# Kernel optimization log

Measured on AMD Instinct MI355X. Metric: run time of the kernel, lower is better.

Reference implementation:

```python
import jax, jax.numpy as jnp
import numpy as np

B, DM, H, W = 4, 192, 48, 48
DI = 2 * DM          # d_inner = d_expand (ssm_ratio=ssm_rank_ratio=2)
K, N, R = 4, 16, 12  # directions, d_state, dt_rank=ceil(192/16)
L = H * W
EPS = 1e-5


def setup_inputs() -> dict:
    key = jax.random.key(0)
    ks = jax.random.split(key, 10)
    f = lambda k, s, sc: (sc * jax.random.normal(k, s)).astype(jnp.float32)
    return {
        "x": jax.random.normal(ks[0], (B, DM, H, W), jnp.float32),
        "in_proj_w": f(ks[1], (2 * DI, DM), 0.05),        # Conv2d 1x1, bias=False
        "conv_w": f(ks[2], (DI, 1, 3, 3), 0.1),           # depthwise 3x3
        "conv_b": f(ks[3], (DI,), 0.1),
        "x_proj_weight": f(ks[4], (K, R + 2 * N, DI), 0.05),
        "dt_projs_weight": f(ks[5], (K, DI, R), 0.1),
        "dt_projs_bias": f(ks[6], (K, DI), 0.5),
        "A_logs": f(ks[7], (K * DI, N), 0.5),
        "Ds": jnp.ones((K * DI,), jnp.float32),
        "ln_w": jnp.ones((DI,), jnp.float32),
        "ln_b": jnp.zeros((DI,), jnp.float32),
        "out_proj_w": f(ks[8], (DM, DI), 0.05),           # Conv2d 1x1, bias=False
    }


def selective_scan(u, delta, A, Bs, Cs, Ds):
    # u, delta: (B,K,D,L); A: (K,D,N); Bs, Cs: (B,K,N,L); Ds: (K,D)
    uT = jnp.moveaxis(u, -1, 0)
    dT = jnp.moveaxis(delta, -1, 0)
    BT = jnp.moveaxis(Bs, -1, 0)
    CT = jnp.moveaxis(Cs, -1, 0)
    h0 = jnp.zeros(u.shape[:3] + (A.shape[-1],), u.dtype)  # (B,K,D,N)

    def step(h, inp):
        u_l, d_l, B_l, C_l = inp  # (B,K,D),(B,K,D),(B,K,N),(B,K,N)
        dA = jnp.exp(d_l[..., None] * A)                    # (B,K,D,N)
        h = h * dA + (d_l * u_l)[..., None] * B_l[:, :, None, :]
        y = jnp.einsum("bkdn,bkn->bkd", h, C_l)
        return h, y

    _, ys = jax.lax.scan(step, h0, (uT, dT, BT, CT))       # ys: (L,B,K,D)
    ys = jnp.moveaxis(ys, 0, -1)                            # (B,K,D,L)
    return ys + u * Ds[None, :, :, None]


def _forward(x, in_proj_w, conv_w, conv_b, x_proj_weight, dt_projs_weight,
             dt_projs_bias, A_logs, Ds, ln_w, ln_b, out_proj_w):
    # in_proj (1x1 conv) -> split x / z; z branch gets exact GELU
    xz = jnp.einsum("od,bdhw->bohw", in_proj_w, x)
    xc, z = jnp.split(xz, 2, axis=1)
    z1 = jax.nn.gelu(z, approximate=False)
    # depthwise 3x3 conv + GELU
    xc = jax.lax.conv_general_dilated(
        xc, conv_w, (1, 1), "SAME",
        feature_group_count=DI,
        dimension_numbers=("NCHW", "OIHW", "NCHW"),
    ) + conv_b[None, :, None, None]
    xc = jax.nn.gelu(xc, approximate=False)
    # CrossScan: row-major, col-major, and their reversals -> (B,K,D,L)
    x0 = xc.reshape(B, DI, L)
    x1 = jnp.swapaxes(xc, 2, 3).reshape(B, DI, L)
    xs = jnp.stack([x0, x1, x0[..., ::-1], x1[..., ::-1]], axis=1)
    # per-direction projections
    x_dbl = jnp.einsum("bkdl,kcd->bkcl", xs, x_proj_weight)
    dts, Bs, Cs = jnp.split(x_dbl, [R, R + N], axis=2)      # (B,K,R,L),(B,K,N,L)x2
    dts = jnp.einsum("bkrl,kdr->bkdl", dts, dt_projs_weight)
    delta = jax.nn.softplus(dts + dt_projs_bias[None, :, :, None])
    A = -jnp.exp(A_logs.reshape(K, DI, N))
    ys = selective_scan(xs, delta, A, Bs, Cs, Ds.reshape(K, DI))
    # CrossMerge: un-flip, fold col-major branch back to row-major
    y02 = ys[:, 0] + ys[:, 2, :, ::-1]
    y13 = ys[:, 1] + ys[:, 3, :, ::-1]
    y = y02 + jnp.swapaxes(y13.reshape(B, DI, W, H), 2, 3).reshape(B, DI, L)
    # out_norm (LayerNorm over channel) in (B,H,W,D)
    y = y.reshape(B, DI, H, W).transpose(0, 2, 3, 1)
    mu = y.mean(-1, keepdims=True)
    var = ((y - mu) ** 2).mean(-1, keepdims=True)
    y = (y - mu) / jnp.sqrt(var + EPS) * ln_w + ln_b
    # gate with z, out_proj 1x1
    y = y.transpose(0, 3, 1, 2) * z1
    return jnp.einsum("od,bdhw->bohw", out_proj_w, y)


def reference(x, in_proj_w, conv_w, conv_b, x_proj_weight, dt_projs_weight,
              dt_projs_bias, A_logs, Ds, ln_w, ln_b, out_proj_w):
    return _forward(x, in_proj_w, conv_w, conv_b, x_proj_weight,
                    dt_projs_weight, dt_projs_bias, A_logs, Ds,
                    ln_w, ln_b, out_proj_w)
```

## Files before the change

kernel.cpp:

```cpp
#include <hip/hip_runtime.h>
#include <math.h>

#define BQ 4
#define DM 192
#define DI 384
#define HH 48
#define WW 48
#define LL 2304
#define KK 4
#define NN 16
#define RR 12
#define CH 48
#define CLEN 48

#define LOG2E 1.4426950408889634f

typedef short v8s __attribute__((ext_vector_type(8)));
typedef float v4f __attribute__((ext_vector_type(4)));

__device__ __forceinline__ float gelu_exact(float x) {
    return 0.5f * x * (1.0f + erff(x * 0.7071067811865476f));
}

__device__ __forceinline__ float softplus_f(float x) {
    return fmaxf(x, 0.0f) + log1pf(expf(-fabsf(x)));
}

__device__ __forceinline__ int pos_for(int k, int l) {
    if (k == 0) return l;
    if (k == 1) { return (l % HH) * WW + (l / HH); }
    if (k == 2) return (LL - 1) - l;
    int j = (LL - 1) - l;
    return (j % HH) * WW + (j / HH);
}

__device__ __forceinline__ int pt_of(int p) {
    return (p % 48) * 48 + p / 48;
}

__device__ __forceinline__ float fexp2(float x) {
    return __builtin_amdgcn_exp2f(x);
}

__device__ __forceinline__ short f2bf(float x) {
    unsigned u = __float_as_uint(x);
    unsigned r = (u + 0x7FFFu + ((u >> 16) & 1u)) >> 16;
    return (short)r;
}

template<int CTRL>
__device__ __forceinline__ float dpp_movf(float v) {
    return __int_as_float(__builtin_amdgcn_update_dpp(
        0, __float_as_int(v), CTRL, 0xF, 0xF, true));
}

__global__ __launch_bounds__(256) void k_prep_w(const float* __restrict__ ipw,
                                                const float* __restrict__ opw,
                                                const float* __restrict__ xpw,
                                                short* __restrict__ wibf,
                                                short* __restrict__ owbf,
                                                short* __restrict__ wpbf) {
    int i = blockIdx.x * 256 + threadIdx.x;
    if (i < 147456)       wibf[i] = f2bf(ipw[i]);
    else if (i < 221184)  owbf[i - 147456] = f2bf(opw[i - 147456]);
    else if (i < 288768)  wpbf[i - 221184] = f2bf(xpw[i - 221184]);
    else                  wpbf[67584 + (i - 288768)] = 0;
}

__global__ __launch_bounds__(256) void k_prep_xT(const float* __restrict__ x,
                                                 short* __restrict__ xTbf) {
    __shared__ float T[32][33];
    int blk = blockIdx.x;
    int dt = blk % 6;
    int lt = (blk / 6) % 72;
    int b  = blk / (6 * 72);
    int d0 = dt * 32, l0 = lt * 32;
    int tx = threadIdx.x & 31, ty = threadIdx.x >> 5;
    #pragma unroll
    for (int i = 0; i < 4; ++i) {
        int dd = ty + 8 * i;
        T[dd][tx] = x[(size_t)(b * DM + d0 + dd) * LL + l0 + tx];
    }
    __syncthreads();
    #pragma unroll
    for (int i = 0; i < 4; ++i) {
        int ll = ty + 8 * i;
        xTbf[(size_t)(b * LL + l0 + ll) * DM + d0 + tx] = f2bf(T[tx][ll]);
    }
}

__global__ __launch_bounds__(256) void k_inproj_mfma(
    const short* __restrict__ xTbf,
    const short* __restrict__ wibf,
    float* __restrict__ xcz)
{
    __shared__ short sA[128 * 40];
    __shared__ short sB[64 * 40];
    int o0 = blockIdx.x * 64;
    int l0 = blockIdx.y * 128;
    int b  = blockIdx.z;
    int tid = threadIdx.x;
    int lane = tid & 63, wid = tid >> 6;
    int n = lane & 15, quad = lane >> 4;

    v4f acc[2][4];
    #pragma unroll
    for (int i = 0; i < 2; ++i)
        #pragma unroll
        for (int j = 0; j < 4; ++j) acc[i][j] = (v4f){0.f, 0.f, 0.f, 0.f};

    for (int kc = 0; kc < 192; kc += 32) {
        for (int i = tid; i < 512; i += 256) {
            int row = i >> 2, seg = i & 3;
            *(v8s*)&sA[row * 40 + seg * 8] =
                *(const v8s*)(xTbf + (size_t)(b * LL + l0 + row) * DM + kc + seg * 8);
        }
        {
            int row = tid >> 2, seg = tid & 3;
            *(v8s*)&sB[row * 40 + seg * 8] =
                *(const v8s*)(wibf + (size_t)(o0 + row) * DM + kc + seg * 8);
        }
        __syncthreads();
        v8s a0 = *(v8s*)&sA[(wid * 32 + n) * 40 + quad * 8];
        v8s a1 = *(v8s*)&sA[(wid * 32 + 16 + n) * 40 + quad * 8];
        #pragma unroll
        for (int os = 0; os < 4; ++os) {
            v8s bv = *(v8s*)&sB[(os * 16 + n) * 40 + quad * 8];
            acc[0][os] = __builtin_amdgcn_mfma_f32_16x16x32_bf16(a0, bv, acc[0][os], 0, 0, 0);
            acc[1][os] = __builtin_amdgcn_mfma_f32_16x16x32_bf16(a1, bv, acc[1][os], 0, 0, 0);
        }
        __syncthreads();
    }
    bool zhalf = (o0 >= DI);
    #pragma unroll
    for (int ls = 0; ls < 2; ++ls)
        #pragma unroll
        for (int os = 0; os < 4; ++os) {
            int o = o0 + os * 16 + n;
            #pragma unroll
            for (int r = 0; r < 4; ++r) {
                int l = l0 + wid * 32 + ls * 16 + quad * 4 + r;
                float v = acc[ls][os][r];
                xcz[(size_t)(b * LL + l) * 768 + o] = zhalf ? gelu_exact(v) : v;
            }
        }
}

__global__ __launch_bounds__(384) void k_dwconv(const float* __restrict__ xcz,
                                                const float* __restrict__ cw,
                                                const float* __restrict__ cb,
                                                float* __restrict__ xcT,
                                                short* __restrict__ xcTbf) {
    int blk = blockIdx.x;
    int seg = blk & 3;
    int bh = blk >> 2;
    int b = bh / HH, h = bh % HH;
    int d = threadIdx.x;
    int w0 = seg * 12;
    const float* in = xcz + (size_t)b * LL * 768 + d;
    float w9[9];
    #pragma unroll
    for (int i = 0; i < 9; ++i) w9[i] = cw[d * 9 + i];
    float bias = cb[d];
    bool hm = h > 0, hp = h < HH - 1;
    int r0 = (h - 1) * WW, r1 = h * WW, r2 = (h + 1) * WW;
    float c00, c01, c02, c10, c11, c12, c20, c21, c22;
    bool wl = (w0 > 0);
    c00 = (hm && wl) ? in[(size_t)(r0 + w0 - 1) * 768] : 0.f;
    c10 = wl ? in[(size_t)(r1 + w0 - 1) * 768] : 0.f;
    c20 = (hp && wl) ? in[(size_t)(r2 + w0 - 1) * 768] : 0.f;
    c01 = hm ? in[(size_t)(r0 + w0) * 768] : 0.f;
    c11 = in[(size_t)(r1 + w0) * 768];
    c21 = hp ? in[(size_t)(r2 + w0) * 768] : 0.f;
    c02 = hm ? in[(size_t)(r0 + w0 + 1) * 768] : 0.f;
    c12 = in[(size_t)(r1 + w0 + 1) * 768];
    c22 = hp ? in[(size_t)(r2 + w0 + 1) * 768] : 0.f;
    #pragma unroll
    for (int wi = 0; wi < 12; ++wi) {
        int w = w0 + wi;
        float s = bias
            + w9[0] * c00 + w9[1] * c01 + w9[2] * c02
            + w9[3] * c10 + w9[4] * c11 + w9[5] * c12
            + w9[6] * c20 + w9[7] * c21 + w9[8] * c22;
        float v = gelu_exact(s);
        size_t row = (size_t)(b * LL + h * WW + w);
        xcT[row * DI + d] = v;
        xcTbf[row * DI + d] = f2bf(v);
        c00 = c01; c01 = c02; c10 = c11; c11 = c12; c20 = c21; c21 = c22;
        int wn = w + 2;
        bool okw = wn < WW;
        c02 = (hm && okw) ? in[(size_t)(r0 + wn) * 768] : 0.f;
        c12 = okw ? in[(size_t)(r1 + wn) * 768] : 0.f;
        c22 = (hp && okw) ? in[(size_t)(r2 + wn) * 768] : 0.f;
    }
}

__global__ __launch_bounds__(256) void k_xproj_mfma(
    const short* __restrict__ xcTbf,
    const short* __restrict__ wpbf,
    float* __restrict__ dts,
    float* __restrict__ Bsb,
    float* __restrict__ Csb)
{
    __shared__ short sA[128 * 40];
    __shared__ short sB[64 * 40];
    int o0 = blockIdx.x * 64;
    int l0 = blockIdx.y * 128;
    int b  = blockIdx.z;
    int tid = threadIdx.x;
    int lane = tid & 63, wid = tid >> 6;
    int n = lane & 15, quad = lane >> 4;

    v4f acc[2][4];
    #pragma unroll
    for (int i = 0; i < 2; ++i)
        #pragma unroll
        for (int j = 0; j < 4; ++j) acc[i][j] = (v4f){0.f, 0.f, 0.f, 0.f};

    for (int kc = 0; kc < DI; kc += 32) {
        for (int i = tid; i < 512; i += 256) {
            int row = i >> 2, seg = i & 3;
            *(v8s*)&sA[row * 40 + seg * 8] =
                *(const v8s*)(xcTbf + (size_t)(b * LL + l0 + row) * DI + kc + seg * 8);
        }
        {
            int row = tid >> 2, seg = tid & 3;
            *(v8s*)&sB[row * 40 + seg * 8] =
                *(const v8s*)(wpbf + (size_t)(o0 + row) * DI + kc + seg * 8);
        }
        __syncthreads();
        v8s a0 = *(v8s*)&sA[(wid * 32 + n) * 40 + quad * 8];
        v8s a1 = *(v8s*)&sA[(wid * 32 + 16 + n) * 40 + quad * 8];
        #pragma unroll
        for (int os = 0; os < 4; ++os) {
            v8s bv = *(v8s*)&sB[(os * 16 + n) * 40 + quad * 8];
            acc[0][os] = __builtin_amdgcn_mfma_f32_16x16x32_bf16(a0, bv, acc[0][os], 0, 0, 0);
            acc[1][os] = __builtin_amdgcn_mfma_f32_16x16x32_bf16(a1, bv, acc[1][os], 0, 0, 0);
        }
        __syncthreads();
    }
    #pragma unroll
    for (int ls = 0; ls < 2; ++ls)
        #pragma unroll
        for (int os = 0; os < 4; ++os) {
            int c_all = o0 + os * 16 + n;
            if (c_all >= 176) continue;
            int k = c_all / 44;
            int c = c_all - k * 44;
            int bk = b * 4 + k;
            #pragma unroll
            for (int r = 0; r < 4; ++r) {
                int lp = l0 + wid * 32 + ls * 16 + quad * 4 + r;
                int lk = (k == 0) ? lp
                       : (k == 1) ? pt_of(lp)
                       : (k == 2) ? (LL - 1 - lp)
                                  : (LL - 1 - pt_of(lp));
                float v = acc[ls][os][r];
                size_t base = (size_t)bk * LL + lk;
                if (c < RR)           dts[base * RR + c] = v;
                else if (c < RR + NN) Bsb[base * NN + (c - RR)] = v;
                else                  Csb[base * NN + (c - RR - NN)] = v;
            }
        }
}

__global__ __launch_bounds__(256) void k_scan_pass1(
    const float* __restrict__ xcT,
    const float* __restrict__ dts,
    const float* __restrict__ Bsb,
    const float* __restrict__ Csb,
    const float* __restrict__ dtw_g,
    const float* __restrict__ dtb_g,
    const float* __restrict__ Alogs,
    const float* __restrict__ Ds_g,
    float* __restrict__ Sbuf,
    float* __restrict__ hstin,
    float* __restrict__ yk)
{
    __shared__ float sB[CLEN * 16];
    __shared__ float sC[CLEN * 16];
    __shared__ float sDts[CLEN * 12];
    __shared__ float sDel[CLEN * 64];
    __shared__ float sU[CLEN * 64];

    int blk = blockIdx.x;
    int dblk = blk % 6;
    int tmp = blk / 6;
    int c = tmp % CH;
    int bk = tmp / CH;
    int k = bk & 3, b = bk >> 2;
    int tid = threadIdx.x;
    int l0 = c * CLEN;

    {
        const float4* Bg = (const float4*)(Bsb + ((size_t)bk * LL + l0) * NN);
        const float4* Cg = (const float4*)(Csb + ((size_t)bk * LL + l0) * NN);
        if (tid < CLEN * 4) {
            ((float4*)sB)[tid] = Bg[tid];
            ((float4*)sC)[tid] = Cg[tid];
        }
        const float4* Dg = (const float4*)(dts + ((size_t)bk * LL + l0) * RR);
        for (int i = tid; i < CLEN * 3; i += 256)
            ((float4*)sDts)[i] = Dg[i];
    }
    {
        const float* xb = xcT + (size_t)b * LL * DI + dblk * 64;
        #pragma unroll
        for (int it = 0; it < 3; ++it) {
            int i = it * 256 + tid;
            int l = i >> 4, f4 = i & 15;
            int pos = pos_for(k, l0 + l);
            ((float4*)sU)[l * 16 + f4] = *(const float4*)(xb + (size_t)pos * DI + f4 * 4);
        }
    }
    __syncthreads();
    {
        int dl = tid & 63, lset = tid >> 6;
        int dd = dblk * 64 + dl;
        int kdq = k * DI + dd;
        float dtbv = dtb_g[kdq];
        float w12[12];
        {
            const float4* p = (const float4*)(dtw_g + (size_t)kdq * RR);
            float4 a0 = p[0], a1 = p[1], a2 = p[2];
            w12[0]=a0.x; w12[1]=a0.y; w12[2]=a0.z;  w12[3]=a0.w;
            w12[4]=a1.x; w12[5]=a1.y; w12[6]=a1.z;  w12[7]=a1.w;
            w12[8]=a2.x; w12[9]=a2.y; w12[10]=a2.z; w12[11]=a2.w;
        }
        #pragma unroll
        for (int j = 0; j < 12; ++j) {
            int l = lset * 12 + j;
            const float* dp = sDts + l * 12;
            float acc = dtbv;
            #pragma unroll
            for (int r = 0; r < 12; ++r) acc += dp[r] * w12[r];
            sDel[l * 64 + dl] = softplus_f(acc);
        }
    }
    __syncthreads();

    int lane = tid & 63, wv = tid >> 6;
    int q = lane & 3;
    int d16 = lane >> 2;
    int dl = wv * 16 + d16;
    int d = dblk * 64 + dl;
    int kd = k * DI + d;
    int n0 = q << 2;

    float4 Al = *(const float4*)(Alogs + (size_t)kd * NN + n0);
    float A2[4] = { -expf(Al.x) * LOG2E, -expf(Al.y) * LOG2E,
                    -expf(Al.z) * LOG2E, -expf(Al.w) * LOG2E };
    float Dv = Ds_g[kd];
    float* Sc = Sbuf + ((size_t)bk * LL + l0 + q) * DI + d;
    float* yc = yk   + ((size_t)bk * LL + l0 + q) * DI + d;

    float h0 = 0.f, h1 = 0.f, h2 = 0.f, h3 = 0.f;
    float td = 0.f;
    float yhold = 0.f, Shold = 0.f;

    #pragma unroll
    for (int l = 0; l < CLEN; ++l) {
        float delta = sDel[l * 64 + dl];
        float ub_b  = sU[l * 64 + dl];
        td += delta;
        float du = delta * ub_b;
        float4 B4 = *(const float4*)&sB[l * 16 + n0];
        h0 = h0 * fexp2(delta * A2[0]) + du * B4.x;
        h1 = h1 * fexp2(delta * A2[1]) + du * B4.y;
        h2 = h2 * fexp2(delta * A2[2]) + du * B4.z;
        h3 = h3 * fexp2(delta * A2[3]) + du * B4.w;
        float4 C4 = *(const float4*)&sC[l * 16 + n0];
        float yp = h0 * C4.x + h1 * C4.y + h2 * C4.z + h3 * C4.w;
        yp += dpp_movf<0xB1>(yp);
        yp += dpp_movf<0x4E>(yp);
        float yf = yp + ub_b * Dv;
        if (q == (l & 3)) { yhold = yf; Shold = td; }
        if ((l & 3) == 3) {
            *yc = yhold; *Sc = Shold;
            yc += 4 * DI; Sc += 4 * DI;
        }
    }

    float4 h4; h4.x = h0; h4.y = h1; h4.z = h2; h4.w = h3;
    *(float4*)(hstin + ((size_t)(bk * CH + c) * DI + d) * NN + n0) = h4;
}

__global__ __launch_bounds__(256) void k_scan_combine(
    float* __restrict__ hstin,
    const float* __restrict__ Sbuf,
    const float* __restrict__ Alogs)
{
    int t = blockIdx.x * 256 + threadIdx.x;
    int n = t & 15;
    int d = (t >> 4) % DI;
    int bk = t / (DI * NN);
    int k = bk & 3;
    float A2 = -expf(Alogs[(size_t)(k * DI + d) * NN + n]) * LOG2E;
    float h = 0.f;
    for (int c = 0; c < CH; ++c) {
        size_t rb = (size_t)(bk * CH + c) * DI + d;
        float hend = hstin[rb * NN + n];
        hstin[rb * NN + n] = h;
        float St = Sbuf[((size_t)bk * LL + c * CLEN + CLEN - 1) * DI + d];
        h = fexp2(A2 * St) * h + hend;
    }
}

__global__ __launch_bounds__(256) void k_corr(
    const float* __restrict__ Csb,
    const float* __restrict__ Sbuf,
    const float* __restrict__ hin,
    const float* __restrict__ Alogs,
    float* __restrict__ yk)
{
    __shared__ float sC[CLEN * 16];
    __shared__ float sS[CLEN * 64];

    int blk = blockIdx.x;
    int dblk = blk % 6;
    int tmp = blk / 6;
    int c = tmp % CH;
    if (c == 0) return;
    int bk = tmp / CH;
    int k = bk & 3;
    int tid = threadIdx.x;
    int l0 = c * CLEN;

    {
        const float4* Cg = (const float4*)(Csb + ((size_t)bk * LL + l0) * NN);
        if (tid < CLEN * 4) ((float4*)sC)[tid] = Cg[tid];
        const float* Sg = Sbuf + ((size_t)bk * LL + l0) * DI + dblk * 64;
        #pragma unroll
        for (int it = 0; it < 3; ++it) {
            int i = it * 256 + tid;
            int l = i >> 4, f4 = i & 15;
            ((float4*)sS)[l * 16 + f4] = *(const float4*)(Sg + (size_t)l * DI + f4 * 4);
        }
    }
    __syncthreads();

    int lane = tid & 63, wv = tid >> 6;
    int q = lane & 3;
    int d16 = lane >> 2;
    int dl = wv * 16 + d16;
    int d = dblk * 64 + dl;
    int kd = k * DI + d;
    int n0 = q << 2;

    float4 Al = *(const float4*)(Alogs + (size_t)kd * NN + n0);
    float A2[4] = { -expf(Al.x) * LOG2E, -expf(Al.y) * LOG2E,
                    -expf(Al.z) * LOG2E, -expf(Al.w) * LOG2E };
    float4 H4 = *(const float4*)(hin + ((size_t)(bk * CH + c) * DI + d) * NN + n0);
    float* yc = yk + ((size_t)bk * LL + l0 + q) * DI + d;

    float ychold = 0.f;
    #pragma unroll
    for (int l = 0; l < CLEN; ++l) {
        float S = sS[l * 64 + dl];
        float4 C4 = *(const float4*)&sC[l * 16 + n0];
        float yv = C4.x * fexp2(A2[0] * S) * H4.x
                 + C4.y * fexp2(A2[1] * S) * H4.y
                 + C4.z * fexp2(A2[2] * S) * H4.z
                 + C4.w * fexp2(A2[3] * S) * H4.w;
        yv += dpp_movf<0xB1>(yv);
        yv += dpp_movf<0x4E>(yv);
        if (q == (l & 3)) ychold = yv;
        if ((l & 3) == 3) {
            *yc += ychold;
            yc += 4 * DI;
        }
    }
}

__global__ __launch_bounds__(384) void k_merge_ln_gate(
    const float* __restrict__ yk,
    const float* __restrict__ xcz,
    const float* __restrict__ lnw,
    const float* __restrict__ lnb,
    short* __restrict__ gbufb)
{
    int pg = blockIdx.x;
    int b = pg / LL;
    int pos = pg % LL;
    int d = threadIdx.x;
    int pt = (pos % 48) * 48 + pos / 48;

    const float* y0 = yk + ((size_t)(b * 4 + 0) * LL + pos) * DI;
    const float* y1 = yk + ((size_t)(b * 4 + 1) * LL + pt) * DI;
    const float* y2 = yk + ((size_t)(b * 4 + 2) * LL + (LL - 1 - pos)) * DI;
    const float* y3 = yk + ((size_t)(b * 4 + 3) * LL + (LL - 1 - pt)) * DI;
    float v = y0[d] + y1[d] + y2[d] + y3[d];

    float s = v, qq = v * v;
    #pragma unroll
    for (int o = 32; o >= 1; o >>= 1) {
        s += __shfl_xor(s, o, 64);
        qq += __shfl_xor(qq, o, 64);
    }
    __shared__ float ssum[6], sqq[6];
    int lane = d & 63, w = d >> 6;
    if (lane == 0) { ssum[w] = s; sqq[w] = qq; }
    __syncthreads();
    float ts = 0.f, tq = 0.f;
    #pragma unroll
    for (int i = 0; i < 6; ++i) { ts += ssum[i]; tq += sqq[i]; }
    float mu = ts / (float)DI;
    float var = tq / (float)DI - mu * mu;
    float inv = rsqrtf(var + 1e-5f);
    float y = (v - mu) * inv * lnw[d] + lnb[d];
    float z = xcz[(size_t)pg * 768 + DI + d];
    gbufb[(size_t)pg * DI + d] = f2bf(y * z);
}

__global__ __launch_bounds__(256) void k_outproj_mfma(
    const short* __restrict__ gbufb,
    const short* __restrict__ owbf,
    float* __restrict__ out)
{
    __shared__ short sA[128 * 40];
    __shared__ short sB[64 * 40];
    int o0 = blockIdx.x * 64;
    int l0 = blockIdx.y * 128;
    int b  = blockIdx.z;
    int tid = threadIdx.x;
    int lane = tid & 63, wid = tid >> 6;
    int n = lane & 15, quad = lane >> 4;

    v4f acc[2][4];
    #pragma unroll
    for (int i = 0; i < 2; ++i)
        #pragma unroll
        for (int j = 0; j < 4; ++j) acc[i][j] = (v4f){0.f, 0.f, 0.f, 0.f};

    for (int kc = 0; kc < DI; kc += 32) {
        for (int i = tid; i < 512; i += 256) {
            int row = i >> 2, seg = i & 3;
            *(v8s*)&sA[row * 40 + seg * 8] =
                *(const v8s*)(gbufb + (size_t)(b * LL + l0 + row) * DI + kc + seg * 8);
        }
        {
            int row = tid >> 2, seg = tid & 3;
            *(v8s*)&sB[row * 40 + seg * 8] =
                *(const v8s*)(owbf + (size_t)(o0 + row) * DI + kc + seg * 8);
        }
        __syncthreads();
        v8s a0 = *(v8s*)&sA[(wid * 32 + n) * 40 + quad * 8];
        v8s a1 = *(v8s*)&sA[(wid * 32 + 16 + n) * 40 + quad * 8];
        #pragma unroll
        for (int os = 0; os < 4; ++os) {
            v8s bv = *(v8s*)&sB[(os * 16 + n) * 40 + quad * 8];
            acc[0][os] = __builtin_amdgcn_mfma_f32_16x16x32_bf16(a0, bv, acc[0][os], 0, 0, 0);
            acc[1][os] = __builtin_amdgcn_mfma_f32_16x16x32_bf16(a1, bv, acc[1][os], 0, 0, 0);
        }
        __syncthreads();
    }
    #pragma unroll
    for (int ls = 0; ls < 2; ++ls)
        #pragma unroll
        for (int os = 0; os < 4; ++os) {
            int o = o0 + os * 16 + n;
            #pragma unroll
            for (int r = 0; r < 4; ++r) {
                int l = l0 + wid * 32 + ls * 16 + quad * 4 + r;
                out[(size_t)(b * DM + o) * LL + l] = acc[ls][os][r];
            }
        }
}

extern "C" void kernel_launch(void* const* d_in, const int* in_sizes, int n_in,
                              void* d_out, int out_size, void* d_ws, size_t ws_size,
                              hipStream_t stream) {
    (void)in_sizes; (void)n_in; (void)out_size; (void)ws_size;
    const float* x      = (const float*)d_in[0];
    const float* ipw    = (const float*)d_in[1];
    const float* cw     = (const float*)d_in[2];
    const float* cb     = (const float*)d_in[3];
    const float* xpw    = (const float*)d_in[4];
    const float* dtw    = (const float*)d_in[5];
    const float* dtb    = (const float*)d_in[6];
    const float* Alogs  = (const float*)d_in[7];
    const float* Ds     = (const float*)d_in[8];
    const float* lnw    = (const float*)d_in[9];
    const float* lnb    = (const float*)d_in[10];
    const float* opw    = (const float*)d_in[11];
    float* out = (float*)d_out;

    float* wsf = (float*)d_ws;
    const size_t XCZ = (size_t)BQ * LL * 768;
    const size_t SZ  = (size_t)BQ * DI * LL;
    const size_t DTS = (size_t)BQ * KK * LL * RR;
    const size_t BCS = (size_t)BQ * KK * LL * NN;
    const size_t SBF = (size_t)BQ * KK * LL * DI;
    const size_t HST = (size_t)BQ * KK * CH * DI * NN;

    float* xcz   = wsf;
    float* xcT   = xcz + XCZ;
    float* dts   = xcT + SZ;
    float* Bsb   = dts + DTS;
    float* Csb   = Bsb + BCS;
    float* Sbuf  = Csb + BCS;
    float* hstin = Sbuf + SBF;
    float* yk    = hstin + HST;
    short* xTbf  = (short*)(yk + SBF);
    short* wibf  = xTbf + (size_t)BQ * LL * DM;
    short* owbf  = wibf + 768 * 192;
    short* wpbf  = owbf + 192 * 384;
    short* gbufb = (short*)Sbuf;
    short* xcTbf = (short*)yk;

    k_prep_w<<<1152, 256, 0, stream>>>(ipw, opw, xpw, wibf, owbf, wpbf);
    k_prep_xT<<<BQ * 72 * 6, 256, 0, stream>>>(x, xTbf);
    k_inproj_mfma<<<dim3(12, 18, BQ), 256, 0, stream>>>(xTbf, wibf, xcz);
    k_dwconv<<<BQ * HH * 4, 384, 0, stream>>>(xcz, cw, cb, xcT, xcTbf);
    k_xproj_mfma<<<dim3(3, 18, BQ), 256, 0, stream>>>(xcTbf, wpbf, dts, Bsb, Csb);

    k_scan_pass1<<<BQ * KK * CH * 6, 256, 0, stream>>>(
        xcT, dts, Bsb, Csb, dtw, dtb, Alogs, Ds, Sbuf, hstin, yk);
    k_scan_combine<<<(BQ * KK * DI * NN) / 256, 256, 0, stream>>>(
        hstin, Sbuf, Alogs);
    k_corr<<<BQ * KK * CH * 6, 256, 0, stream>>>(Csb, Sbuf, hstin, Alogs, yk);
    k_merge_ln_gate<<<BQ * LL, 384, 0, stream>>>(yk, xcz, lnw, lnb, gbufb);

    k_outproj_mfma<<<dim3(3, 18, BQ), 256, 0, stream>>>(gbufb, owbf, out);
}
```

Before: 304.2 us.

## Recompute delta prefix sums in correction pass instead of storing full S buffer

The scan pass no longer writes the per-position cumulative delta buffer (B*K*L*DI floats). It stores only each chunk's final sum, which the combine kernel reads. The correction kernel instead reloads the small dt rows, recomputes delta via the dt projection and softplus, and keeps a running sum, trading a large global write and read for extra compute. The two prep kernels are also merged into one launch to save a kernel launch.

```diff
diff --git a/kernel.cpp b/kernel.cpp
--- a/kernel.cpp
+++ b/kernel.cpp
@@ -54,23 +54,24 @@
         0, __float_as_int(v), CTRL, 0xF, 0xF, true));
 }
 
-__global__ __launch_bounds__(256) void k_prep_w(const float* __restrict__ ipw,
-                                                const float* __restrict__ opw,
-                                                const float* __restrict__ xpw,
-                                                short* __restrict__ wibf,
-                                                short* __restrict__ owbf,
-                                                short* __restrict__ wpbf) {
-    int i = blockIdx.x * 256 + threadIdx.x;
-    if (i < 147456)       wibf[i] = f2bf(ipw[i]);
-    else if (i < 221184)  owbf[i - 147456] = f2bf(opw[i - 147456]);
-    else if (i < 288768)  wpbf[i - 221184] = f2bf(xpw[i - 221184]);
-    else                  wpbf[67584 + (i - 288768)] = 0;
-}
-
-__global__ __launch_bounds__(256) void k_prep_xT(const float* __restrict__ x,
-                                                 short* __restrict__ xTbf) {
+__global__ __launch_bounds__(256) void k_prep(const float* __restrict__ ipw,
+                                              const float* __restrict__ opw,
+                                              const float* __restrict__ xpw,
+                                              const float* __restrict__ x,
+                                              short* __restrict__ wibf,
+                                              short* __restrict__ owbf,
+                                              short* __restrict__ wpbf,
+                                              short* __restrict__ xTbf) {
     __shared__ float T[32][33];
-    int blk = blockIdx.x;
+    if (blockIdx.x < 1152) {
+        int i = blockIdx.x * 256 + threadIdx.x;
+        if (i < 147456)       wibf[i] = f2bf(ipw[i]);
+        else if (i < 221184)  owbf[i - 147456] = f2bf(opw[i - 147456]);
+        else if (i < 288768)  wpbf[i - 221184] = f2bf(xpw[i - 221184]);
+        else                  wpbf[67584 + (i - 288768)] = 0;
+        return;
+    }
+    int blk = blockIdx.x - 1152;
     int dt = blk % 6;
     int lt = (blk / 6) % 72;
     int b  = blk / (6 * 72);
@@ -273,7 +274,7 @@
     const float* __restrict__ dtb_g,
     const float* __restrict__ Alogs,
     const float* __restrict__ Ds_g,
-    float* __restrict__ Sbuf,
+    float* __restrict__ Sfin,
     float* __restrict__ hstin,
     float* __restrict__ yk)
 {
@@ -351,12 +352,11 @@
     float A2[4] = { -expf(Al.x) * LOG2E, -expf(Al.y) * LOG2E,
                     -expf(Al.z) * LOG2E, -expf(Al.w) * LOG2E };
     float Dv = Ds_g[kd];
-    float* Sc = Sbuf + ((size_t)bk * LL + l0 + q) * DI + d;
-    float* yc = yk   + ((size_t)bk * LL + l0 + q) * DI + d;
+    float* yc = yk + ((size_t)bk * LL + l0 + q) * DI + d;
 
     float h0 = 0.f, h1 = 0.f, h2 = 0.f, h3 = 0.f;
     float td = 0.f;
-    float yhold = 0.f, Shold = 0.f;
+    float yhold = 0.f;
 
     #pragma unroll
     for (int l = 0; l < CLEN; ++l) {
@@ -374,20 +374,21 @@
         yp += dpp_movf<0xB1>(yp);
         yp += dpp_movf<0x4E>(yp);
         float yf = yp + ub_b * Dv;
-        if (q == (l & 3)) { yhold = yf; Shold = td; }
+        if (q == (l & 3)) yhold = yf;
         if ((l & 3) == 3) {
-            *yc = yhold; *Sc = Shold;
-            yc += 4 * DI; Sc += 4 * DI;
+            *yc = yhold;
+            yc += 4 * DI;
         }
     }
 
     float4 h4; h4.x = h0; h4.y = h1; h4.z = h2; h4.w = h3;
     *(float4*)(hstin + ((size_t)(bk * CH + c) * DI + d) * NN + n0) = h4;
+    if (q == 0) Sfin[(size_t)(bk * CH + c) * DI + d] = td;
 }
 
 __global__ __launch_bounds__(256) void k_scan_combine(
     float* __restrict__ hstin,
-    const float* __restrict__ Sbuf,
+    const float* __restrict__ Sfin,
     const float* __restrict__ Alogs)
 {
     int t = blockIdx.x * 256 + threadIdx.x;
@@ -401,20 +402,22 @@
         size_t rb = (size_t)(bk * CH + c) * DI + d;
         float hend = hstin[rb * NN + n];
         hstin[rb * NN + n] = h;
-        float St = Sbuf[((size_t)bk * LL + c * CLEN + CLEN - 1) * DI + d];
-        h = fexp2(A2 * St) * h + hend;
+        h = fexp2(A2 * Sfin[rb]) * h + hend;
     }
 }
 
 __global__ __launch_bounds__(256) void k_corr(
     const float* __restrict__ Csb,
-    const float* __restrict__ Sbuf,
+    const float* __restrict__ dts,
+    const float* __restrict__ dtw_g,
+    const float* __restrict__ dtb_g,
     const float* __restrict__ hin,
     const float* __restrict__ Alogs,
     float* __restrict__ yk)
 {
     __shared__ float sC[CLEN * 16];
-    __shared__ float sS[CLEN * 64];
+    __shared__ float sDts[CLEN * 12];
+    __shared__ float sDel[CLEN * 64];
 
     int blk = blockIdx.x;
     int dblk = blk % 6;
@@ -429,12 +432,32 @@
     {
         const float4* Cg = (const float4*)(Csb + ((size_t)bk * LL + l0) * NN);
         if (tid < CLEN * 4) ((float4*)sC)[tid] = Cg[tid];
-        const float* Sg = Sbuf + ((size_t)bk * LL + l0) * DI + dblk * 64;
-        #pragma unroll
-        for (int it = 0; it < 3; ++it) {
-            int i = it * 256 + tid;
-            int l = i >> 4, f4 = i & 15;
-            ((float4*)sS)[l * 16 + f4] = *(const float4*)(Sg + (size_t)l * DI + f4 * 4);
+        const float4* Dg = (const float4*)(dts + ((size_t)bk * LL + l0) * RR);
+        for (int i = tid; i < CLEN * 3; i += 256)
+            ((float4*)sDts)[i] = Dg[i];
+    }
+    __syncthreads();
+    {
+        int dl = tid & 63, lset = tid >> 6;
+        int dd = dblk * 64 + dl;
+        int kdq = k * DI + dd;
+        float dtbv = dtb_g[kdq];
+        float w12[12];
+        {
+            const float4* p = (const float4*)(dtw_g + (size_t)kdq * RR);
+            float4 a0 = p[0], a1 = p[1], a2 = p[2];
+            w12[0]=a0.x; w12[1]=a0.y; w12[2]=a0.z;  w12[3]=a0.w;
+            w12[4]=a1.x; w12[5]=a1.y; w12[6]=a1.z;  w12[7]=a1.w;
+            w12[8]=a2.x; w12[9]=a2.y; w12[10]=a2.z; w12[11]=a2.w;
+        }
+        #pragma unroll
+        for (int j = 0; j < 12; ++j) {
+            int l = lset * 12 + j;
+            const float* dp = sDts + l * 12;
+            float acc = dtbv;
+            #pragma unroll
+            for (int r = 0; r < 12; ++r) acc += dp[r] * w12[r];
+            sDel[l * 64 + dl] = softplus_f(acc);
         }
     }
     __syncthreads();
@@ -453,15 +476,16 @@
     float4 H4 = *(const float4*)(hin + ((size_t)(bk * CH + c) * DI + d) * NN + n0);
     float* yc = yk + ((size_t)bk * LL + l0 + q) * DI + d;
 
+    float td = 0.f;
     float ychold = 0.f;
     #pragma unroll
     for (int l = 0; l < CLEN; ++l) {
-        float S = sS[l * 64 + dl];
+        td += sDel[l * 64 + dl];
         float4 C4 = *(const float4*)&sC[l * 16 + n0];
-        float yv = C4.x * fexp2(A2[0] * S) * H4.x
-                 + C4.y * fexp2(A2[1] * S) * H4.y
-                 + C4.z * fexp2(A2[2] * S) * H4.z
-                 + C4.w * fexp2(A2[3] * S) * H4.w;
+        float yv = C4.x * fexp2(A2[0] * td) * H4.x
+                 + C4.y * fexp2(A2[1] * td) * H4.y
+                 + C4.z * fexp2(A2[2] * td) * H4.z
+                 + C4.w * fexp2(A2[3] * td) * H4.w;
         yv += dpp_movf<0xB1>(yv);
         yv += dpp_movf<0x4E>(yv);
         if (q == (l & 3)) ychold = yv;
@@ -598,27 +622,29 @@
     float* dts   = xcT + SZ;
     float* Bsb   = dts + DTS;
     float* Csb   = Bsb + BCS;
-    float* Sbuf  = Csb + BCS;
-    float* hstin = Sbuf + SBF;
+    float* Sreg  = Csb + BCS;
+    float* hstin = Sreg + SBF;
     float* yk    = hstin + HST;
     short* xTbf  = (short*)(yk + SBF);
     short* wibf  = xTbf + (size_t)BQ * LL * DM;
     short* owbf  = wibf + 768 * 192;
     short* wpbf  = owbf + 192 * 384;
-    short* gbufb = (short*)Sbuf;
+    float* Sfin  = (float*)(wpbf + 192 * 384);
+    short* gbufb = (short*)Sreg;
     short* xcTbf = (short*)yk;
 
-    k_prep_w<<<1152, 256, 0, stream>>>(ipw, opw, xpw, wibf, owbf, wpbf);
-    k_prep_xT<<<BQ * 72 * 6, 256, 0, stream>>>(x, xTbf);
+    k_prep<<<1152 + BQ * 72 * 6, 256, 0, stream>>>(
+        ipw, opw, xpw, x, wibf, owbf, wpbf, xTbf);
     k_inproj_mfma<<<dim3(12, 18, BQ), 256, 0, stream>>>(xTbf, wibf, xcz);
     k_dwconv<<<BQ * HH * 4, 384, 0, stream>>>(xcz, cw, cb, xcT, xcTbf);
     k_xproj_mfma<<<dim3(3, 18, BQ), 256, 0, stream>>>(xcTbf, wpbf, dts, Bsb, Csb);
 
     k_scan_pass1<<<BQ * KK * CH * 6, 256, 0, stream>>>(
-        xcT, dts, Bsb, Csb, dtw, dtb, Alogs, Ds, Sbuf, hstin, yk);
+        xcT, dts, Bsb, Csb, dtw, dtb, Alogs, Ds, Sfin, hstin, yk);
     k_scan_combine<<<(BQ * KK * DI * NN) / 256, 256, 0, stream>>>(
-        hstin, Sbuf, Alogs);
-    k_corr<<<BQ * KK * CH * 6, 256, 0, stream>>>(Csb, Sbuf, hstin, Alogs, yk);
+        hstin, Sfin, Alogs);
+    k_corr<<<BQ * KK * CH * 6, 256, 0, stream>>>(
+        Csb, dts, dtw, dtb, hstin, Alogs, yk);
     k_merge_ln_gate<<<BQ * LL, 384, 0, stream>>>(yk, xcz, lnw, lnb, gbufb);
 
     k_outproj_mfma<<<dim3(3, 18, BQ), 256, 0, stream>>>(gbufb, owbf, out);
```

After: 331.0 us. 8.8% more time.
